# Kernel tuning notes

Measured on AMD Instinct MI355X. Metric: run time of the kernel, lower is better.

The kernel has to match this reference:

```python
import jax, jax.numpy as jnp
import numpy as np
from jax import lax

DIST_THRESH = 180.0
ATT_THRESH = 0.05


def setup_inputs() -> dict:
    key = jax.random.key(0)
    ks = jax.random.split(key, 6)
    B, N, H, W = 16, 512, 25, 25
    F, Fh = H * W, int(H * W * 1.5)  # 625, 937
    x4 = jax.random.normal(ks[0], (B, N, H, W), dtype=jnp.float32) * 0.25
    attention = jax.random.uniform(ks[1], (B, N, 1, 1), dtype=jnp.float32)
    W1 = jax.random.normal(ks[2], (2, F, Fh), dtype=jnp.float32) * (1.0 / np.sqrt(F))
    b1 = jnp.zeros((Fh,), dtype=jnp.float32)
    W2 = jax.random.normal(ks[3], (2, Fh, F), dtype=jnp.float32) * (1.0 / np.sqrt(Fh))
    b2 = jnp.zeros((F,), dtype=jnp.float32)
    return {"x4": x4, "attention": attention, "W1": W1, "b1": b1, "W2": W2, "b2": b2}


def _build_adjacency(X, att):
    """X: [B,N,F] node features, att: [B,N]. Returns thresholded adjacency [B,N,N]."""
    B, N, F = X.shape
    # pairwise L1 distances, row-by-row scan to avoid materializing [B,N,N,F]
    Xs = jnp.swapaxes(X, 0, 1)  # [N,B,F]

    def row(_, xi):  # xi: [B,F]
        d = jnp.sum(jnp.abs(xi[:, None, :] - X), axis=-1)  # [B,N]
        return None, d

    _, D = lax.scan(row, None, Xs)          # [N,B,N]
    D = jnp.swapaxes(D, 0, 1)               # [B,N,N]
    att_d = jnp.abs(att[:, :, None] - att[:, None, :])  # [B,N,N]
    A = ((D <= DIST_THRESH) & (att_d <= ATT_THRESH)).astype(jnp.float32)
    # original only fills i<j and j<i, diagonal stays 0
    A = A * (1.0 - jnp.eye(N, dtype=jnp.float32))
    return A


def _process_graph(A):
    """A + I, then row-normalize by inverse degree (D^-1 (A+I))."""
    N = A.shape[1]
    A = A + jnp.eye(N, dtype=A.dtype)
    deg = jnp.sum(A, axis=-1)               # [B,N]
    dinv = jnp.where(deg > 0, 1.0 / deg, 0.0)
    return dinv[:, :, None] * A


def _cheb_conv(x, L, Wk, b):
    """ChebConv with K=2 over dense normalized graph L: T0=x, T1=Lx."""
    t1 = jnp.einsum('bij,bjf->bif', L, x)
    return jnp.einsum('bnf,fo->bno', x, Wk[0]) + jnp.einsum('bnf,fo->bno', t1, Wk[1]) + b


def reference(x4, attention, W1, b1, W2, b2):
    B, N, H, W = x4.shape
    X = x4.reshape(B, N, H * W)             # [B,N,625] flow_x
    att = attention[:, :, 0, 0]             # [B,N]
    A = _build_adjacency(X, att)
    L = _process_graph(A)
    h = jax.nn.relu(_cheb_conv(X, L, W1, b1))   # [B,N,937]
    out = jax.nn.relu(_cheb_conv(h, L, W2, b2))  # [B,N,625]
    return out
```

## Files before the change

kernel.cpp:

```cpp
#include <hip/hip_runtime.h>
#include <stdint.h>

typedef uint16_t u16;
typedef __attribute__((ext_vector_type(4))) float f32x4;
typedef __attribute__((ext_vector_type(4))) unsigned short us4;
typedef __attribute__((ext_vector_type(8))) unsigned short us8;

#define NB   16
#define NN   512
#define FF   625
#define FH   937
#define ROWS 8192
#define KS1  1280
#define KS2  1920
#define NP1  1024
#define NP2  640
#define F4   160

using frag_ab = __attribute__((ext_vector_type(8))) short;
using frag_cd = __attribute__((ext_vector_type(4))) float;

__device__ __forceinline__ u16 f32_bf16(float f) {
  union { float f; uint32_t u; } x; x.f = f;
  uint32_t r = x.u + 0x7fffu + ((x.u >> 16) & 1u);
  return (u16)(r >> 16);
}
__device__ __forceinline__ float bf16_f32(u16 u) {
  union { uint32_t u; float f; } x; x.u = ((uint32_t)u) << 16;
  return x.f;
}
__device__ __forceinline__ void gload_lds16(const void* g, void* l) {
  __builtin_amdgcn_global_load_lds((__attribute__((address_space(1))) void*)g,
                                   (__attribute__((address_space(3))) void*)l,
                                   16, 0, 0);
}
__device__ __forceinline__ int swiz_row(int blk) {
  return ((blk & 7) << 10) | (blk >> 3);
}

__global__ __launch_bounds__(256) void prep(
    const float* __restrict__ x4, const float* __restrict__ W1,
    const float* __restrict__ W2, f32x4* __restrict__ Xpad,
    u16* __restrict__ Xcat, u16* __restrict__ W1t, u16* __restrict__ W2t)
{
  const int blk = blockIdx.x;
  if (blk < 5120) {
    const int idx = blk * 256 + threadIdx.x;
    if (idx >= ROWS * F4) return;
    const int row = idx / F4;
    const int k4 = idx - row * F4;
    f32x4 v; us4 o;
    #pragma unroll
    for (int t = 0; t < 4; ++t) {
      const int f = k4 * 4 + t;
      float x = (f < FF) ? x4[(size_t)row * FF + f] : 0.f;
      v[t] = x; o[t] = f32_bf16(x);
    }
    Xpad[idx] = v;
    *(us4*)(Xcat + (size_t)row * KS1 + k4 * 4) = o;
  } else if (blk < 6400) {
    __shared__ float tile[32][33];
    const int bb = blk - 5120;
    const int kt = bb % 40, nt = bb / 40;
    const int tx = threadIdx.x & 31, ty = threadIdx.x >> 5;
    #pragma unroll
    for (int r = 0; r < 4; ++r) {
      int k = kt * 32 + ty + r * 8;
      int n = nt * 32 + tx;
      float v = 0.f;
      int c = -1, kk = 0;
      if (k < 625) { c = 0; kk = k; }
      else if (k >= 640 && k < 1265) { c = 1; kk = k - 640; }
      if (c >= 0 && n < FH) v = W1[((size_t)c * 625 + kk) * FH + n];
      tile[ty + r * 8][tx] = v;
    }
    __syncthreads();
    #pragma unroll
    for (int r = 0; r < 4; ++r) {
      int n = nt * 32 + ty + r * 8;
      int k = kt * 32 + tx;
      W1t[(size_t)n * KS1 + k] = f32_bf16(tile[tx][ty + r * 8]);
    }
  } else {
    __shared__ float tile[32][33];
    const int bb = blk - 6400;
    const int kt = bb % 60, nt = bb / 60;
    const int tx = threadIdx.x & 31, ty = threadIdx.x >> 5;
    #pragma unroll
    for (int r = 0; r < 4; ++r) {
      int k = kt * 32 + ty + r * 8;
      int n = nt * 32 + tx;
      float v = 0.f;
      int c = -1, kk = 0;
      if (k < 937) { c = 0; kk = k; }
      else if (k >= 960 && k < 1897) { c = 1; kk = k - 960; }
      if (c >= 0 && n < FF) v = W2[((size_t)c * 937 + kk) * FF + n];
      tile[ty + r * 8][tx] = v;
    }
    __syncthreads();
    #pragma unroll
    for (int r = 0; r < 4; ++r) {
      int n = nt * 32 + ty + r * 8;
      int k = kt * 32 + tx;
      W2t[(size_t)n * KS2 + k] = f32_bf16(tile[tx][ty + r * 8]);
    }
  }
}

__global__ __launch_bounds__(256) void build_graph(
    const f32x4* __restrict__ Xpad,
    const float* __restrict__ att,
    u16* __restrict__ Xcat,
    u16* __restrict__ nbr,
    int* __restrict__ degbuf,
    float* __restrict__ invbuf)
{
  __shared__ float att_sh[512];
  __shared__ f32x4 Xi4[F4];
  __shared__ u16 cand[512];
  __shared__ u16 accj[512];
  __shared__ f32x4 wsum[4][F4];
  __shared__ int ncand, nacc;

  const int tid = threadIdx.x;
  const int row = swiz_row(blockIdx.x);
  const int b = row >> 9;
  const int i = row & 511;
  const f32x4* Xb4 = Xpad + (size_t)b * NN * F4;

  att_sh[tid]       = att[b * NN + tid];
  att_sh[tid + 256] = att[b * NN + tid + 256];
  if (tid < F4) Xi4[tid] = Xb4[(size_t)i * F4 + tid];
  if (tid == 0) { ncand = 0; nacc = 0; }
  __syncthreads();

  const float ai = att_sh[i];
  for (int j = tid; j < NN; j += 256) {
    if (j != i && fabsf(ai - att_sh[j]) <= 0.05f) {
      int p = atomicAdd(&ncand, 1);
      cand[p] = (u16)j;
    }
  }
  __syncthreads();

  const int lane = tid & 63;
  const int wave = tid >> 6;
  const int nc = ncand;

  const f32x4 zero = {0.f, 0.f, 0.f, 0.f};
  const f32x4 a0 = Xi4[lane];
  const f32x4 a1 = Xi4[64 + lane];
  const f32x4 a2 = (lane < 32) ? Xi4[128 + lane] : zero;
  f32x4 s0 = zero, s1 = zero, s2 = zero;

  f32x4 x0 = zero, x1 = zero, x2 = zero;
  if (wave < nc) {
    const f32x4* Xj = Xb4 + (size_t)cand[wave] * F4;
    x0 = Xj[lane]; x1 = Xj[64 + lane]; x2 = (lane < 32) ? Xj[128 + lane] : zero;
  }
  for (int c = wave; c < nc; c += 4) {
    const int cn = (c + 4 < nc) ? c + 4 : c;
    const f32x4* Xn = Xb4 + (size_t)cand[cn] * F4;
    const f32x4 y0 = Xn[lane];
    const f32x4 y1 = Xn[64 + lane];
    const f32x4 y2 = (lane < 32) ? Xn[128 + lane] : zero;

    const f32x4 d0 = a0 - x0, d1 = a1 - x1, d2 = a2 - x2;
    float p = 0.f;
    #pragma unroll
    for (int t = 0; t < 4; ++t)
      p += fabsf(d0[t]) + fabsf(d1[t]) + fabsf(d2[t]);
    #pragma unroll
    for (int off = 32; off; off >>= 1) p += __shfl_xor(p, off, 64);
    if (p <= 180.0f) {
      s0 += x0; s1 += x1; s2 += x2;
      if (lane == 0) { int q = atomicAdd(&nacc, 1); accj[q] = cand[c]; }
    }
    x0 = y0; x1 = y1; x2 = y2;
  }
  wsum[wave][lane] = s0;
  wsum[wave][64 + lane] = s1;
  if (lane < 32) wsum[wave][128 + lane] = s2;
  __syncthreads();

  const int na = nacc;
  const float inv = 1.0f / (float)(na + 1);
  for (int c = tid; c < na; c += 256) nbr[(size_t)row * 512 + c] = accj[c];
  if (tid == 0) { degbuf[row] = na; invbuf[row] = inv; }

  for (int k = tid; k < F4; k += 256) {
    f32x4 t = Xi4[k];
    #pragma unroll
    for (int w = 0; w < 4; ++w) t += wsum[w][k];
    us4 o;
    #pragma unroll
    for (int s = 0; s < 4; ++s) o[s] = f32_bf16(t[s] * inv);
    *(us4*)(Xcat + (size_t)row * KS1 + 640 + k * 4) = o;
  }
}

__global__ __launch_bounds__(256) void gather2(
    u16* __restrict__ hcat,
    const u16* __restrict__ nbr,
    const int* __restrict__ degbuf,
    const float* __restrict__ invbuf)
{
  __shared__ u16 accj[512];
  __shared__ float hsum[2][8][120];

  const int tid = threadIdx.x;
  const int row = swiz_row(blockIdx.x);
  const int b = row >> 9;
  const int na = degbuf[row];
  const float inv = invbuf[row];
  for (int c = tid; c < na; c += 256) accj[c] = nbr[(size_t)row * 512 + c];
  __syncthreads();

  const int g = tid >> 7;
  const int slot = tid & 127;
  const u16* hbat = hcat + (size_t)b * NN * KS2;

  float s[8] = {0,0,0,0,0,0,0,0};
  if (slot < 120) {
    for (int c = g; c < na; c += 2) {
      const us8 hv = *(const us8*)(hbat + (size_t)accj[c] * KS2 + slot * 8);
      #pragma unroll
      for (int t = 0; t < 8; ++t) s[t] += bf16_f32(hv[t]);
    }
    #pragma unroll
    for (int t = 0; t < 8; ++t) hsum[g][t][slot] = s[t];
  }
  __syncthreads();

  if (tid < 23) hcat[(size_t)row * KS2 + FH + tid] = 0;

  const u16* hrow = hcat + (size_t)row * KS2;
  for (int k = tid; k < 120; k += 256) {
    const us8 hv = *(const us8*)(hrow + k * 8);
    us8 o;
    #pragma unroll
    for (int t = 0; t < 8; ++t) {
      const int col = k * 8 + t;
      float v = (bf16_f32(hv[t]) + hsum[0][t][k] + hsum[1][t][k]) * inv;
      o[t] = (col < FH) ? f32_bf16(v) : (u16)0;
    }
    *(us8*)(hcat + (size_t)row * KS2 + 960 + k * 8) = o;
  }
}

template <int KS, int NTILE, int NREAL, int LDC, bool OUT_BF16>
__global__ __launch_bounds__(256) void gemm_bt64(
    const u16* __restrict__ A, const u16* __restrict__ Bt,
    const float* __restrict__ bias, void* __restrict__ C)
{
  constexpr int NI = NTILE / 32;
  constexpr int BR = NTILE / 32;
  __shared__ __align__(16) u16 Ash[128 * 64];
  __shared__ __align__(16) u16 Bsh[NTILE * 64];

  const int tid  = threadIdx.x;
  const int lane = tid & 63;
  const int wave = tid >> 6;
  const int wm = wave & 1, wn = wave >> 1;
  const int q = lane >> 4, l16 = lane & 15;
  const int x = blockIdx.x;
  const int mt = ((x & 7) << 3) | (x >> 3);
  const int m0 = mt * 128;
  const int n0 = blockIdx.y * NTILE;

  const u16* pa[4]; const u16* pb[BR];
  #pragma unroll
  for (int r = 0; r < 4; ++r) {
    const int ci = r * 256 + tid;
    const int row = ci >> 3, cpos = ci & 7;
    pa[r] = A + (size_t)(m0 + row) * KS + (cpos ^ (row & 7)) * 8;
  }
  #pragma unroll
  for (int r = 0; r < BR; ++r) {
    const int ci = r * 256 + tid;
    const int row = ci >> 3, cpos = ci & 7;
    pb[r] = Bt + (size_t)(n0 + row) * KS + (cpos ^ (row & 7)) * 8;
  }
  const int wbase = (tid & 192) * 8;

  const frag_ab* fA[4][2]; const frag_ab* fB[NI][2];
  #pragma unroll
  for (int mi = 0; mi < 4; ++mi) {
    const int row = wm * 64 + mi * 16 + l16;
    fA[mi][0] = (const frag_ab*)&Ash[row * 64 + ((q    ) ^ (l16 & 7)) * 8];
    fA[mi][1] = (const frag_ab*)&Ash[row * 64 + ((q + 4) ^ (l16 & 7)) * 8];
  }
  #pragma unroll
  for (int ni = 0; ni < NI; ++ni) {
    const int row = wn * (NTILE / 2) + ni * 16 + l16;
    fB[ni][0] = (const frag_ab*)&Bsh[row * 64 + ((q    ) ^ (l16 & 7)) * 8];
    fB[ni][1] = (const frag_ab*)&Bsh[row * 64 + ((q + 4) ^ (l16 & 7)) * 8];
  }

  frag_cd acc[4][NI] = {};

  constexpr int KT = KS / 64;
  for (int kt = 0; kt < KT; ++kt) {
    __syncthreads();
    #pragma unroll
    for (int r = 0; r < 4; ++r) {
      gload_lds16(pa[r], &Ash[r * 2048 + wbase]);
      pa[r] += 64;
    }
    #pragma unroll
    for (int r = 0; r < BR; ++r) {
      gload_lds16(pb[r], &Bsh[r * 2048 + wbase]);
      pb[r] += 64;
    }
    __syncthreads();

    #pragma unroll
    for (int kk = 0; kk < 2; ++kk) {
      frag_ab av[4], bv[NI];
      #pragma unroll
      for (int mi = 0; mi < 4; ++mi) av[mi] = *fA[mi][kk];
      #pragma unroll
      for (int ni = 0; ni < NI; ++ni) bv[ni] = *fB[ni][kk];
      #pragma unroll
      for (int mi = 0; mi < 4; ++mi)
        #pragma unroll
        for (int ni = 0; ni < NI; ++ni)
          acc[mi][ni] = __builtin_amdgcn_mfma_f32_16x16x32_bf16(
              av[mi], bv[ni], acc[mi][ni], 0, 0, 0);
    }
  }

  #pragma unroll
  for (int ni = 0; ni < NI; ++ni) {
    const int col = n0 + wn * (NTILE / 2) + ni * 16 + l16;
    const bool ok = (col < NREAL);
    const float bvv = ok ? bias[col] : 0.f;
    #pragma unroll
    for (int mi = 0; mi < 4; ++mi) {
      #pragma unroll
      for (int r = 0; r < 4; ++r) {
        const int rowg = m0 + wm * 64 + mi * 16 + q * 4 + r;
        float v = acc[mi][ni][r] + bvv;
        v = fmaxf(v, 0.f);
        if (ok) {
          if (OUT_BF16)
            ((u16*)C)[(size_t)rowg * LDC + col] = f32_bf16(v);
          else
            ((float*)C)[(size_t)rowg * LDC + col] = v;
        }
      }
    }
  }
}

extern "C" void kernel_launch(void* const* d_in, const int* in_sizes, int n_in,
                              void* d_out, int out_size, void* d_ws, size_t ws_size,
                              hipStream_t stream) {
  const float* x4  = (const float*)d_in[0];
  const float* att = (const float*)d_in[1];
  const float* W1  = (const float*)d_in[2];
  const float* b1  = (const float*)d_in[3];
  const float* W2  = (const float*)d_in[4];
  const float* b2  = (const float*)d_in[5];
  float* out = (float*)d_out;

  char* ws = (char*)d_ws;
  f32x4* Xpad = (f32x4*)ws; ws += (size_t)ROWS * F4 * 16;
  u16* Xcat = (u16*)ws;  ws += (size_t)ROWS * KS1 * 2;
  u16* hcat = (u16*)ws;  ws += (size_t)ROWS * KS2 * 2;
  u16* W1t  = (u16*)ws;  ws += (size_t)NP1 * KS1 * 2;
  u16* W2t  = (u16*)ws;  ws += (size_t)NP2 * KS2 * 2;
  u16* nbr  = (u16*)ws;  ws += (size_t)ROWS * 512 * 2;
  int*   deg = (int*)ws;   ws += (size_t)ROWS * 4;
  float* inv = (float*)ws; ws += (size_t)ROWS * 4;

  prep<<<dim3(7600), 256, 0, stream>>>(x4, W1, W2, Xpad, Xcat, W1t, W2t);
  build_graph<<<dim3(ROWS), 256, 0, stream>>>(Xpad, att, Xcat, nbr, deg, inv);
  gemm_bt64<KS1, 128, FH, KS2, true><<<dim3(64, NP1 / 128), 256, 0, stream>>>(
      Xcat, W1t, b1, (void*)hcat);
  gather2<<<dim3(ROWS), 256, 0, stream>>>(hcat, nbr, deg, inv);
  gemm_bt64<KS2, 64, FF, FF, false><<<dim3(64, NP2 / 64), 256, 0, stream>>>(
      hcat, W2t, b2, (void*)out);
}
```

Measured before the change: 241.2 us.

## Replace sparse neighbor gathers with dense bf16 L matrix and MFMA SpMM

Instead of recording neighbor lists and summing neighbor rows with scalar gathers, build_L writes a dense bf16 normalized adjacency L per batch. L·X and L·h then run as batched MFMA GEMMs against transposed feature matrices (a new Xt in prep and a new transpose_h kernel). The distance test now uses half-wave groups of 32 lanes with 8 candidates in flight per block. This trades irregular gather traffic for dense matrix-core work. It adds an extra transpose pass, extra L and transposed-buffer traffic, and rounds the 1/deg weights to bf16.

```diff
diff --git a/kernel.cpp b/kernel.cpp
--- a/kernel.cpp
+++ b/kernel.cpp
@@ -2,6 +2,7 @@
 #include <stdint.h>
 
 typedef uint16_t u16;
+typedef uint32_t u32;
 typedef __attribute__((ext_vector_type(4))) float f32x4;
 typedef __attribute__((ext_vector_type(4))) unsigned short us4;
 typedef __attribute__((ext_vector_type(8))) unsigned short us8;
@@ -13,8 +14,8 @@
 #define ROWS 8192
 #define KS1  1280
 #define KS2  1920
-#define NP1  1024
-#define NP2  640
+#define NPX  640
+#define NPH  960
 #define F4   160
 
 using frag_ab = __attribute__((ext_vector_type(8))) short;
@@ -25,10 +26,6 @@
   uint32_t r = x.u + 0x7fffu + ((x.u >> 16) & 1u);
   return (u16)(r >> 16);
 }
-__device__ __forceinline__ float bf16_f32(u16 u) {
-  union { uint32_t u; float f; } x; x.u = ((uint32_t)u) << 16;
-  return x.f;
-}
 __device__ __forceinline__ void gload_lds16(const void* g, void* l) {
   __builtin_amdgcn_global_load_lds((__attribute__((address_space(1))) void*)g,
                                    (__attribute__((address_space(3))) void*)l,
@@ -41,28 +38,53 @@
 __global__ __launch_bounds__(256) void prep(
     const float* __restrict__ x4, const float* __restrict__ W1,
     const float* __restrict__ W2, f32x4* __restrict__ Xpad,
-    u16* __restrict__ Xcat, u16* __restrict__ W1t, u16* __restrict__ W2t)
+    u16* __restrict__ Xcat, u16* __restrict__ Xt,
+    u16* __restrict__ W1t, u16* __restrict__ W2t)
 {
   const int blk = blockIdx.x;
-  if (blk < 5120) {
-    const int idx = blk * 256 + threadIdx.x;
-    if (idx >= ROWS * F4) return;
-    const int row = idx / F4;
-    const int k4 = idx - row * F4;
-    f32x4 v; us4 o;
-    #pragma unroll
-    for (int t = 0; t < 4; ++t) {
-      const int f = k4 * 4 + t;
-      float x = (f < FF) ? x4[(size_t)row * FF + f] : 0.f;
-      v[t] = x; o[t] = f32_bf16(x);
-    }
-    Xpad[idx] = v;
-    *(us4*)(Xcat + (size_t)row * KS1 + k4 * 4) = o;
-  } else if (blk < 6400) {
+  const int tid = threadIdx.x;
+  if (blk < 4096) {
+    const int xcd = blk & 7, loc = blk >> 3;
+    const int row0 = xcd * 1024 + loc * 2;
+    for (int s = tid; s < 320; s += 256) {
+      const int row = row0 + (s >= 160);
+      const int k4 = (s >= 160) ? s - 160 : s;
+      f32x4 v; us4 o;
+      #pragma unroll
+      for (int t = 0; t < 4; ++t) {
+        const int f = k4 * 4 + t;
+        float x = (f < FF) ? x4[(size_t)row * FF + f] : 0.f;
+        v[t] = x; o[t] = f32_bf16(x);
+      }
+      Xpad[(size_t)row * F4 + k4] = v;
+      *(us4*)(Xcat + (size_t)row * KS1 + k4 * 4) = o;
+    }
+  } else if (blk < 9216) {
     __shared__ float tile[32][33];
-    const int bb = blk - 5120;
+    const int bb = blk - 4096;
+    const int xcd = bb & 7, sub = bb >> 3;
+    const int b = xcd * 2 + sub / 320;
+    const int t = sub % 320;
+    const int ft = t % 20, kt = t / 20;
+    const int tx = tid & 31, ty = tid >> 5;
+    #pragma unroll
+    for (int r = 0; r < 4; ++r) {
+      const int node = kt * 32 + ty + r * 8;
+      const int f = ft * 32 + tx;
+      tile[ty + r * 8][tx] = (f < FF) ? x4[((size_t)b * NN + node) * FF + f] : 0.f;
+    }
+    __syncthreads();
+    #pragma unroll
+    for (int r = 0; r < 4; ++r) {
+      const int f = ft * 32 + ty + r * 8;
+      const int node = kt * 32 + tx;
+      Xt[((size_t)b * NPX + f) * 512 + node] = f32_bf16(tile[tx][ty + r * 8]);
+    }
+  } else if (blk < 10496) {
+    __shared__ float tile[32][33];
+    const int bb = blk - 9216;
     const int kt = bb % 40, nt = bb / 40;
-    const int tx = threadIdx.x & 31, ty = threadIdx.x >> 5;
+    const int tx = tid & 31, ty = tid >> 5;
     #pragma unroll
     for (int r = 0; r < 4; ++r) {
       int k = kt * 32 + ty + r * 8;
@@ -83,9 +105,9 @@
     }
   } else {
     __shared__ float tile[32][33];
-    const int bb = blk - 6400;
+    const int bb = blk - 10496;
     const int kt = bb % 60, nt = bb / 60;
-    const int tx = threadIdx.x & 31, ty = threadIdx.x >> 5;
+    const int tx = tid & 31, ty = tid >> 5;
     #pragma unroll
     for (int r = 0; r < 4; ++r) {
       int k = kt * 32 + ty + r * 8;
@@ -107,19 +129,15 @@
   }
 }
 
-__global__ __launch_bounds__(256) void build_graph(
+__global__ __launch_bounds__(256) void build_L(
     const f32x4* __restrict__ Xpad,
     const float* __restrict__ att,
-    u16* __restrict__ Xcat,
-    u16* __restrict__ nbr,
-    int* __restrict__ degbuf,
-    float* __restrict__ invbuf)
+    u16* __restrict__ L)
 {
   __shared__ float att_sh[512];
   __shared__ f32x4 Xi4[F4];
   __shared__ u16 cand[512];
-  __shared__ u16 accj[512];
-  __shared__ f32x4 wsum[4][F4];
+  __shared__ u16 flag[512];
   __shared__ int ncand, nacc;
 
   const int tid = threadIdx.x;
@@ -131,6 +149,7 @@
   att_sh[tid]       = att[b * NN + tid];
   att_sh[tid + 256] = att[b * NN + tid + 256];
   if (tid < F4) Xi4[tid] = Xb4[(size_t)i * F4 + tid];
+  flag[tid] = 0; flag[tid + 256] = 0;
   if (tid == 0) { ncand = 0; nacc = 0; }
   __syncthreads();
 
@@ -142,116 +161,51 @@
     }
   }
   __syncthreads();
-
-  const int lane = tid & 63;
-  const int wave = tid >> 6;
+  if (tid == 0) flag[i] = 1;
+
+  const int hl = tid & 31;
+  const int hw = tid >> 5;
   const int nc = ncand;
 
-  const f32x4 zero = {0.f, 0.f, 0.f, 0.f};
-  const f32x4 a0 = Xi4[lane];
-  const f32x4 a1 = Xi4[64 + lane];
-  const f32x4 a2 = (lane < 32) ? Xi4[128 + lane] : zero;
-  f32x4 s0 = zero, s1 = zero, s2 = zero;
-
-  f32x4 x0 = zero, x1 = zero, x2 = zero;
-  if (wave < nc) {
-    const f32x4* Xj = Xb4 + (size_t)cand[wave] * F4;
-    x0 = Xj[lane]; x1 = Xj[64 + lane]; x2 = (lane < 32) ? Xj[128 + lane] : zero;
-  }
-  for (int c = wave; c < nc; c += 4) {
-    const int cn = (c + 4 < nc) ? c + 4 : c;
-    const f32x4* Xn = Xb4 + (size_t)cand[cn] * F4;
-    const f32x4 y0 = Xn[lane];
-    const f32x4 y1 = Xn[64 + lane];
-    const f32x4 y2 = (lane < 32) ? Xn[128 + lane] : zero;
-
-    const f32x4 d0 = a0 - x0, d1 = a1 - x1, d2 = a2 - x2;
+  const f32x4 a0 = Xi4[hl];
+  const f32x4 a1 = Xi4[32 + hl];
+  const f32x4 a2 = Xi4[64 + hl];
+  const f32x4 a3 = Xi4[96 + hl];
+  const f32x4 a4 = Xi4[128 + hl];
+
+  for (int c = hw; c < nc; c += 8) {
+    const int j = cand[c];
+    const f32x4* Xj = Xb4 + (size_t)j * F4;
+    const f32x4 d0 = a0 - Xj[hl];
+    const f32x4 d1 = a1 - Xj[32 + hl];
+    const f32x4 d2 = a2 - Xj[64 + hl];
+    const f32x4 d3 = a3 - Xj[96 + hl];
+    const f32x4 d4 = a4 - Xj[128 + hl];
     float p = 0.f;
     #pragma unroll
     for (int t = 0; t < 4; ++t)
-      p += fabsf(d0[t]) + fabsf(d1[t]) + fabsf(d2[t]);
-    #pragma unroll
-    for (int off = 32; off; off >>= 1) p += __shfl_xor(p, off, 64);
-    if (p <= 180.0f) {
-      s0 += x0; s1 += x1; s2 += x2;
-      if (lane == 0) { int q = atomicAdd(&nacc, 1); accj[q] = cand[c]; }
-    }
-    x0 = y0; x1 = y1; x2 = y2;
-  }
-  wsum[wave][lane] = s0;
-  wsum[wave][64 + lane] = s1;
-  if (lane < 32) wsum[wave][128 + lane] = s2;
+      p += fabsf(d0[t]) + fabsf(d1[t]) + fabsf(d2[t]) + fabsf(d3[t]) + fabsf(d4[t]);
+    #pragma unroll
+    for (int off = 16; off; off >>= 1) p += __shfl_xor(p, off, 64);
+    if (hl == 0 && p <= 180.0f) {
+      atomicAdd(&nacc, 1);
+      flag[j] = 1;
+    }
+  }
   __syncthreads();
 
-  const int na = nacc;
-  const float inv = 1.0f / (float)(na + 1);
-  for (int c = tid; c < na; c += 256) nbr[(size_t)row * 512 + c] = accj[c];
-  if (tid == 0) { degbuf[row] = na; invbuf[row] = inv; }
-
-  for (int k = tid; k < F4; k += 256) {
-    f32x4 t = Xi4[k];
-    #pragma unroll
-    for (int w = 0; w < 4; ++w) t += wsum[w][k];
-    us4 o;
-    #pragma unroll
-    for (int s = 0; s < 4; ++s) o[s] = f32_bf16(t[s] * inv);
-    *(us4*)(Xcat + (size_t)row * KS1 + 640 + k * 4) = o;
-  }
-}
-
-__global__ __launch_bounds__(256) void gather2(
-    u16* __restrict__ hcat,
-    const u16* __restrict__ nbr,
-    const int* __restrict__ degbuf,
-    const float* __restrict__ invbuf)
-{
-  __shared__ u16 accj[512];
-  __shared__ float hsum[2][8][120];
-
-  const int tid = threadIdx.x;
-  const int row = swiz_row(blockIdx.x);
-  const int b = row >> 9;
-  const int na = degbuf[row];
-  const float inv = invbuf[row];
-  for (int c = tid; c < na; c += 256) accj[c] = nbr[(size_t)row * 512 + c];
-  __syncthreads();
-
-  const int g = tid >> 7;
-  const int slot = tid & 127;
-  const u16* hbat = hcat + (size_t)b * NN * KS2;
-
-  float s[8] = {0,0,0,0,0,0,0,0};
-  if (slot < 120) {
-    for (int c = g; c < na; c += 2) {
-      const us8 hv = *(const us8*)(hbat + (size_t)accj[c] * KS2 + slot * 8);
-      #pragma unroll
-      for (int t = 0; t < 8; ++t) s[t] += bf16_f32(hv[t]);
-    }
-    #pragma unroll
-    for (int t = 0; t < 8; ++t) hsum[g][t][slot] = s[t];
-  }
-  __syncthreads();
-
-  if (tid < 23) hcat[(size_t)row * KS2 + FH + tid] = 0;
-
-  const u16* hrow = hcat + (size_t)row * KS2;
-  for (int k = tid; k < 120; k += 256) {
-    const us8 hv = *(const us8*)(hrow + k * 8);
-    us8 o;
-    #pragma unroll
-    for (int t = 0; t < 8; ++t) {
-      const int col = k * 8 + t;
-      float v = (bf16_f32(hv[t]) + hsum[0][t][k] + hsum[1][t][k]) * inv;
-      o[t] = (col < FH) ? f32_bf16(v) : (u16)0;
-    }
-    *(us8*)(hcat + (size_t)row * KS2 + 960 + k * 8) = o;
-  }
-}
-
-template <int KS, int NTILE, int NREAL, int LDC, bool OUT_BF16>
-__global__ __launch_bounds__(256) void gemm_bt64(
-    const u16* __restrict__ A, const u16* __restrict__ Bt,
-    const float* __restrict__ bias, void* __restrict__ C)
+  const u16 dv = f32_bf16(1.0f / (float)(nacc + 1));
+  const u32 lo = flag[2 * tid]     ? (u32)dv : 0u;
+  const u32 hi = flag[2 * tid + 1] ? (u32)dv : 0u;
+  *(u32*)(L + (size_t)row * 512 + 2 * tid) = lo | (hi << 16);
+}
+
+template <int KS, int NTILE, int NREAL, int NSTORE, bool RELU, bool BIAS, bool OUT_BF16>
+__device__ __forceinline__ void gemm_core(
+    const u16* __restrict__ At,
+    const u16* __restrict__ Btt,
+    const float* __restrict__ bias, void* __restrict__ C,
+    long crow0, int col0, int ldc)
 {
   constexpr int NI = NTILE / 32;
   constexpr int BR = NTILE / 32;
@@ -263,23 +217,19 @@
   const int wave = tid >> 6;
   const int wm = wave & 1, wn = wave >> 1;
   const int q = lane >> 4, l16 = lane & 15;
-  const int x = blockIdx.x;
-  const int mt = ((x & 7) << 3) | (x >> 3);
-  const int m0 = mt * 128;
-  const int n0 = blockIdx.y * NTILE;
 
   const u16* pa[4]; const u16* pb[BR];
   #pragma unroll
   for (int r = 0; r < 4; ++r) {
     const int ci = r * 256 + tid;
     const int row = ci >> 3, cpos = ci & 7;
-    pa[r] = A + (size_t)(m0 + row) * KS + (cpos ^ (row & 7)) * 8;
+    pa[r] = At + (size_t)row * KS + (cpos ^ (row & 7)) * 8;
   }
   #pragma unroll
   for (int r = 0; r < BR; ++r) {
     const int ci = r * 256 + tid;
     const int row = ci >> 3, cpos = ci & 7;
-    pb[r] = Bt + (size_t)(n0 + row) * KS + (cpos ^ (row & 7)) * 8;
+    pb[r] = Btt + (size_t)row * KS + (cpos ^ (row & 7)) * 8;
   }
   const int wbase = (tid & 192) * 8;
 
@@ -303,15 +253,9 @@
   for (int kt = 0; kt < KT; ++kt) {
     __syncthreads();
     #pragma unroll
-    for (int r = 0; r < 4; ++r) {
-      gload_lds16(pa[r], &Ash[r * 2048 + wbase]);
-      pa[r] += 64;
-    }
-    #pragma unroll
-    for (int r = 0; r < BR; ++r) {
-      gload_lds16(pb[r], &Bsh[r * 2048 + wbase]);
-      pb[r] += 64;
-    }
+    for (int r = 0; r < 4; ++r) { gload_lds16(pa[r], &Ash[r * 2048 + wbase]); pa[r] += 64; }
+    #pragma unroll
+    for (int r = 0; r < BR; ++r) { gload_lds16(pb[r], &Bsh[r * 2048 + wbase]); pb[r] += 64; }
     __syncthreads();
 
     #pragma unroll
@@ -332,24 +276,79 @@
 
   #pragma unroll
   for (int ni = 0; ni < NI; ++ni) {
-    const int col = n0 + wn * (NTILE / 2) + ni * 16 + l16;
+    const int col = col0 + wn * (NTILE / 2) + ni * 16 + l16;
+    if (col >= NSTORE) continue;
     const bool ok = (col < NREAL);
-    const float bvv = ok ? bias[col] : 0.f;
+    float bvv = 0.f;
+    if (BIAS) bvv = ok ? bias[col] : 0.f;
     #pragma unroll
     for (int mi = 0; mi < 4; ++mi) {
       #pragma unroll
       for (int r = 0; r < 4; ++r) {
-        const int rowg = m0 + wm * 64 + mi * 16 + q * 4 + r;
-        float v = acc[mi][ni][r] + bvv;
-        v = fmaxf(v, 0.f);
-        if (ok) {
-          if (OUT_BF16)
-            ((u16*)C)[(size_t)rowg * LDC + col] = f32_bf16(v);
-          else
-            ((float*)C)[(size_t)rowg * LDC + col] = v;
-        }
+        const long rowg = crow0 + wm * 64 + mi * 16 + q * 4 + r;
+        float v = acc[mi][ni][r];
+        if (BIAS) v += bvv;
+        if (RELU) v = fmaxf(v, 0.f);
+        if (!ok) v = 0.f;
+        if (OUT_BF16) ((u16*)C)[rowg * (size_t)ldc + col] = f32_bf16(v);
+        else          ((float*)C)[rowg * (size_t)ldc + col] = v;
       }
     }
+  }
+}
+
+template <int KS, int NTILE, int NREAL, int NSTORE, bool RELU, bool BIAS, bool OUT_BF16>
+__global__ __launch_bounds__(256) void gemm_dense(
+    const u16* __restrict__ A, const u16* __restrict__ Bt,
+    const float* __restrict__ bias, void* __restrict__ C, int ldc)
+{
+  const int x = blockIdx.x;
+  const int mt = ((x & 7) << 3) | (x >> 3);
+  gemm_core<KS, NTILE, NREAL, NSTORE, RELU, BIAS, OUT_BF16>(
+      A + (size_t)mt * 128 * KS, Bt + (size_t)blockIdx.y * NTILE * KS,
+      bias, C, (long)mt * 128, blockIdx.y * NTILE, ldc);
+}
+
+template <int NP>
+__global__ __launch_bounds__(256) void spmm(
+    const u16* __restrict__ L, const u16* __restrict__ Bt,
+    u16* __restrict__ C, int ldc)
+{
+  constexpr int TPB = 4 * (NP / 64);
+  const int blk = blockIdx.x;
+  const int xcd = blk & 7, sub = blk >> 3;
+  const int b = xcd * 2 + sub / TPB;
+  const int t = sub % TPB;
+  const int mt = t & 3, nt = t >> 2;
+  gemm_core<512, 64, NP, NP, false, false, true>(
+      L + ((size_t)b * 512 + mt * 128) * 512,
+      Bt + ((size_t)b * NP + nt * 64) * 512,
+      nullptr, C, (long)b * 512 + mt * 128, nt * 64, ldc);
+}
+
+__global__ __launch_bounds__(256) void transpose_h(
+    const u16* __restrict__ hcat, u16* __restrict__ ht)
+{
+  __shared__ u16 tile[32][34];
+  const int blk = blockIdx.x;
+  const int xcd = blk & 7, sub = blk >> 3;
+  const int b = xcd * 2 + sub / 480;
+  const int t = sub % 480;
+  const int kt = t % 16, nt = t / 16;
+  const int tid = threadIdx.x;
+  const int tx = tid & 31, ty = tid >> 5;
+  #pragma unroll
+  for (int r = 0; r < 4; ++r) {
+    const int node = kt * 32 + ty + r * 8;
+    const int n = nt * 32 + tx;
+    tile[ty + r * 8][tx] = hcat[((size_t)b * NN + node) * KS2 + n];
+  }
+  __syncthreads();
+  #pragma unroll
+  for (int r = 0; r < 4; ++r) {
+    const int n = nt * 32 + ty + r * 8;
+    const int node = kt * 32 + tx;
+    ht[((size_t)b * NPH + n) * 512 + node] = tile[tx][ty + r * 8];
   }
 }
 
@@ -365,20 +364,22 @@
   float* out = (float*)d_out;
 
   char* ws = (char*)d_ws;
-  f32x4* Xpad = (f32x4*)ws; ws += (size_t)ROWS * F4 * 16;
+  f32x4* Xpad = (f32x4*)ws;
+  u16* ht = (u16*)ws;       ws += (size_t)ROWS * F4 * 16;
   u16* Xcat = (u16*)ws;  ws += (size_t)ROWS * KS1 * 2;
   u16* hcat = (u16*)ws;  ws += (size_t)ROWS * KS2 * 2;
-  u16* W1t  = (u16*)ws;  ws += (size_t)NP1 * KS1 * 2;
-  u16* W2t  = (u16*)ws;  ws += (size_t)NP2 * KS2 * 2;
-  u16* nbr  = (u16*)ws;  ws += (size_t)ROWS * 512 * 2;
-  int*   deg = (int*)ws;   ws += (size_t)ROWS * 4;
-  float* inv = (float*)ws; ws += (size_t)ROWS * 4;
-
-  prep<<<dim3(7600), 256, 0, stream>>>(x4, W1, W2, Xpad, Xcat, W1t, W2t);
-  build_graph<<<dim3(ROWS), 256, 0, stream>>>(Xpad, att, Xcat, nbr, deg, inv);
-  gemm_bt64<KS1, 128, FH, KS2, true><<<dim3(64, NP1 / 128), 256, 0, stream>>>(
-      Xcat, W1t, b1, (void*)hcat);
-  gather2<<<dim3(ROWS), 256, 0, stream>>>(hcat, nbr, deg, inv);
-  gemm_bt64<KS2, 64, FF, FF, false><<<dim3(64, NP2 / 64), 256, 0, stream>>>(
-      hcat, W2t, b2, (void*)out);
-}
+  u16* W1t  = (u16*)ws;  ws += (size_t)1024 * KS1 * 2;
+  u16* W2t  = (u16*)ws;  ws += (size_t)640 * KS2 * 2;
+  u16* Lm   = (u16*)ws;  ws += (size_t)NB * 512 * 512 * 2;
+  u16* Xt   = (u16*)ws;  ws += (size_t)NB * NPX * 512 * 2;
+
+  prep<<<dim3(11696), 256, 0, stream>>>(x4, W1, W2, Xpad, Xcat, Xt, W1t, W2t);
+  build_L<<<dim3(ROWS), 256, 0, stream>>>(Xpad, att, Lm);
+  spmm<NPX><<<dim3(640), 256, 0, stream>>>(Lm, Xt, Xcat + NPX, KS1);
+  gemm_dense<KS1, 128, FH, NPH, true, true, true><<<dim3(64, 8), 256, 0, stream>>>(
+      Xcat, W1t, b1, (void*)hcat, KS2);
+  transpose_h<<<dim3(7680), 256, 0, stream>>>(hcat, ht);
+  spmm<NPH><<<dim3(960), 256, 0, stream>>>(Lm, ht, hcat + NPH, KS2);
+  gemm_dense<KS2, 64, FF, FF, true, true, false><<<dim3(64, 10), 256, 0, stream>>>(
+      hcat, W2t, b2, (void*)out, FF);
+}
```

New measurement: 222.2 us. -7.9%, faster.
